# Kernel tuning notes

Hardware: AMD Instinct MI355X
Metric: run time of the kernel (lower is better)

Reference implementation:

```python
import jax, jax.numpy as jnp
import numpy as np

D = 2048       # hidden / input / output width
DEPTH = 9      # infinite_depth (layer default)


def _infinite_layer(x, inf_w, cls_w, cls_b):
    """Faithful vectorized InfiniteNeuralLayer.forward.

    Original per-(sample, j, depth) Python loops build a circulant rotation
    matrix M = cos*I + sin*(shift_down - shift_up) and apply it 3x per depth
    with angles inf_w[depth, j, 0..2]. The rotated state never depends on x,
    so we carry one state row per output index j and scan over the 27 angle
    steps, expressing M @ s as cos*s + sin*(roll(s,1) - roll(s,-1)).
    infinite_biases is unused in the original forward and is omitted.
    """
    dim = x.shape[1]
    classical = x @ cls_w + cls_b                      # [B, dim]
    # angles per j per depth step: (DEPTH, dim_j, 3) -> sequence (DEPTH*3, dim_j)
    angles = jnp.transpose(inf_w[:, :, :3], (0, 2, 1)).reshape(-1, dim)
    init = jnp.full((dim, dim), 1.0 / np.sqrt(dim), dtype=x.dtype)  # [j, state]

    def step(s, a):
        c = jnp.cos(a)[:, None]
        sn = jnp.sin(a)[:, None]
        s_new = c * s + sn * (jnp.roll(s, 1, axis=1) - jnp.roll(s, -1, axis=1))
        return s_new, None

    state, _ = jax.lax.scan(step, init, angles)        # [dim_j, dim]
    p = state[:, 0] ** 2                               # |state[0]|^2 per j
    return jnp.tanh(classical + p[None, :])            # broadcast over batch


def setup_inputs() -> dict:
    key = jax.random.key(0)
    ks = jax.random.split(key, 16)
    s = 0.02  # keep activations in sane range (original uses raw randn)
    f = jax.random.normal
    return {
        "x":      f(ks[0], (2048, D), dtype=jnp.float32),
        "w0":     f(ks[1], (D, D), dtype=jnp.float32) * s,
        "b0":     f(ks[2], (D,), dtype=jnp.float32) * s,
        "w1":     f(ks[3], (D, D), dtype=jnp.float32) * s,
        "b1":     f(ks[4], (D,), dtype=jnp.float32) * s,
        "inf_w1": f(ks[5], (DEPTH, D, D), dtype=jnp.float32),
        "cls_w1": f(ks[6], (D, D), dtype=jnp.float32) * s,
        "cls_b1": f(ks[7], (D,), dtype=jnp.float32) * s,
        "w2":     f(ks[8], (D, D), dtype=jnp.float32) * s,
        "b2":     f(ks[9], (D,), dtype=jnp.float32) * s,
        "inf_w2": f(ks[10], (DEPTH, D, D), dtype=jnp.float32),
        "cls_w2": f(ks[11], (D, D), dtype=jnp.float32) * s,
        "cls_b2": f(ks[12], (D,), dtype=jnp.float32) * s,
        "w3":     f(ks[13], (D, D), dtype=jnp.float32) * s,
        "b3":     f(ks[14], (D,), dtype=jnp.float32) * s,
    }


def reference(x, w0, b0, w1, b1, inf_w1, cls_w1, cls_b1,
              w2, b2, inf_w2, cls_w2, cls_b2, w3, b3):
    h = jax.nn.relu(x @ w0 + b0)
    h = jax.nn.relu(h @ w1 + b1)
    h = _infinite_layer(h, inf_w1, cls_w1, cls_b1)
    h = jax.nn.relu(h @ w2 + b2)
    h = _infinite_layer(h, inf_w2, cls_w2, cls_b2)
    return jax.nn.relu(h @ w3 + b3)
```

## Files before the change

### kernel.cpp

```cpp
#include <hip/hip_runtime.h>
#include <hip/hip_bf16.h>


#define DD 2048
#define DEPTH 9

#define BM 128
#define BN 64
#define BK 32
#define NT (DD / BK)

typedef __attribute__((ext_vector_type(8))) short short8;
typedef __attribute__((ext_vector_type(4))) float f32x4;

__device__ __forceinline__ unsigned short f2bf(float f) {
  unsigned u = __float_as_uint(f);
  u += 0x7FFFu + ((u >> 16) & 1u);
  return (unsigned short)(u >> 16);
}

__global__ __launch_bounds__(256) void prep_kernel(
    const float* __restrict__ w0, const float* __restrict__ w1,
    unsigned short* __restrict__ wts, const float* __restrict__ x,
    unsigned short* __restrict__ xb, const float* __restrict__ infw1,
    const float* __restrict__ infw2, const float* __restrict__ clsb1,
    const float* __restrict__ clsb2, float* __restrict__ padd1,
    float* __restrict__ padd2) {
  int b = blockIdx.x;
  int tid = threadIdx.x;
  if (b < 8192) {
    __shared__ float tile[32][33];
    int z = b >> 12;
    int t = b & 4095;
    const float* src = z ? w1 : w0;
    unsigned short* dst = wts + (size_t)z * DD * DD;
    int bx = (t & 63) * 32;
    int by = (t >> 6) * 32;
    int tx = tid & 31, ty = tid >> 5;
#pragma unroll
    for (int i = ty; i < 32; i += 8)
      tile[i][tx] = src[(size_t)(by + i) * DD + bx + tx];
    __syncthreads();
#pragma unroll
    for (int i = ty; i < 32; i += 8)
      dst[(size_t)(bx + i) * DD + by + tx] = f2bf(tile[tx][i]);
  } else if (b < 12288) {
    int i = (b - 8192) * 256 + tid;
    float4 v = reinterpret_cast<const float4*>(x)[i];
    ushort4 o;
    o.x = f2bf(v.x); o.y = f2bf(v.y); o.z = f2bf(v.z); o.w = f2bf(v.w);
    reinterpret_cast<ushort4*>(xb)[i] = o;
  } else {
    int jj = (b - 12288) * 256 + tid;
    int layer = jj >> 11;
    int j = jj & 2047;
    const float* inf_w = layer ? infw2 : infw1;
    const float* cls_b = layer ? clsb2 : clsb1;
    float* padd = layer ? padd2 : padd1;
    float prod = 1.0f;
#pragma unroll
    for (int d = 0; d < DEPTH; ++d) {
      const float* row = inf_w + ((size_t)d * DD + j) * DD;
      prod *= cosf(row[0]) * cosf(row[1]) * cosf(row[2]);
    }
    padd[j] = cls_b[j] + prod * prod * (1.0f / (float)DD);
  }
}


__device__ __forceinline__ void gload_lds16(const unsigned short* g,
                                            unsigned short* l) {
  __builtin_amdgcn_global_load_lds(
      (const __attribute__((address_space(1))) void*)g,
      (__attribute__((address_space(3))) void*)l, 16, 0, 0);
}

__device__ __forceinline__ void waitv6() {
  asm volatile("s_waitcnt vmcnt(6)" ::: "memory");
}
__device__ __forceinline__ void waitv3() {
  asm volatile("s_waitcnt vmcnt(3)" ::: "memory");
}
__device__ __forceinline__ void waitv0() {
  asm volatile("s_waitcnt vmcnt(0)" ::: "memory");
}

template <int EPI>
__global__ __launch_bounds__(256) void gemm_kernel(
    const unsigned short* __restrict__ A, const unsigned short* __restrict__ Bt,
    const float* __restrict__ bias, unsigned short* __restrict__ Cb,
    float* __restrict__ Cf, const float* __restrict__ tsrc,
    unsigned short* __restrict__ tdst) {
  const int N = DD, K = DD;
  __shared__ __align__(16) unsigned char smem[49152];
  unsigned short* As = (unsigned short*)smem;
  unsigned short* Bs = (unsigned short*)(smem + 4 * BM * BK * 2);

  int tid = threadIdx.x;
  int wid = tid >> 6, lane = tid & 63;
  int wr = wid >> 1, wc = wid & 1;
  int lr = lane & 15;
  int lg = lane >> 4;

  int bid = blockIdx.x;
  int swz = (bid & 7) * 64 + (bid >> 3);
  int bcol = (swz & 31) * BN;
  int brow = (swz >> 5) * BM;

  const unsigned short* Abase = A + (size_t)brow * K;
  const unsigned short* Bbase = Bt + (size_t)bcol * K;

  auto stage = [&](int buf, int tile) {
    int kt = tile * BK;
#pragma unroll
    for (int r = 0; r < 2; ++r) {
      int chunk = r * 256 + tid;
      int row = chunk >> 2;
      int sp = chunk & 3;
      int kof = (sp ^ ((row >> 1) & 3)) * 8;
      gload_lds16(Abase + (size_t)row * K + kt + kof,
                  As + buf * (BM * BK) + (size_t)(r * 256 + wid * 64) * 8);
    }
    {
      int row = tid >> 2;
      int sp = tid & 3;
      int kof = (sp ^ ((row >> 1) & 3)) * 8;
      gload_lds16(Bbase + (size_t)row * K + kt + kof,
                  Bs + buf * (BN * BK) + (size_t)(wid * 64) * 8);
    }
  };

  f32x4 acc[4][2];
#pragma unroll
  for (int i = 0; i < 4; ++i)
#pragma unroll
    for (int j = 0; j < 2; ++j) acc[i][j] = f32x4{0.f, 0.f, 0.f, 0.f};

  auto compute = [&](int buf) {
    short8 a[4], b[2];
#pragma unroll
    for (int mt = 0; mt < 4; ++mt) {
      int row = wr * 64 + mt * 16 + lr;
      int slot = lg ^ ((row >> 1) & 3);
      a[mt] = *reinterpret_cast<const short8*>(
          &As[buf * (BM * BK) + row * BK + slot * 8]);
    }
#pragma unroll
    for (int nt = 0; nt < 2; ++nt) {
      int row = wc * 32 + nt * 16 + lr;
      int slot = lg ^ ((row >> 1) & 3);
      b[nt] = *reinterpret_cast<const short8*>(
          &Bs[buf * (BN * BK) + row * BK + slot * 8]);
    }
    __builtin_amdgcn_s_setprio(1);
#pragma unroll
    for (int mt = 0; mt < 4; ++mt)
#pragma unroll
      for (int nt = 0; nt < 2; ++nt)
        acc[mt][nt] = __builtin_amdgcn_mfma_f32_16x16x32_bf16(
            a[mt], b[nt], acc[mt][nt], 0, 0, 0);
    __builtin_amdgcn_s_setprio(0);
  };

  auto step = [&](int buf, int pf_tile, int wcase) {
    if (wcase == 0) waitv6();
    else if (wcase == 1) waitv3();
    else waitv0();
    __builtin_amdgcn_s_barrier();
    __builtin_amdgcn_sched_barrier(0);
    compute(buf);
    if (pf_tile < NT) stage(pf_tile & 3, pf_tile);
  };

  stage(0, 0); stage(1, 1); stage(2, 2);
#pragma unroll 1
  for (int i = 0; i < 15; ++i) {
    int t = 4 * i;
    step(0, t + 3, 0);
    step(1, t + 4, 0);
    step(2, t + 5, 0);
    step(3, t + 6, 0);
  }
  step(0, 63, 0);
  step(1, NT, 0);
  step(2, NT, 1);
  step(3, NT, 2);

  {
    float* et = reinterpret_cast<float*>(smem);
    __syncthreads();
#pragma unroll
    for (int nt = 0; nt < 2; ++nt) {
      int colb = wc * 32 + nt * 16 + lr;
      float bs = bias[bcol + colb];
#pragma unroll
      for (int mt = 0; mt < 4; ++mt) {
#pragma unroll
        for (int i = 0; i < 4; ++i) {
          int rowb = wr * 64 + mt * 16 + lg * 4 + i;
          float v = acc[mt][nt][i] + bs;
          v = (EPI == 1) ? tanhf(v) : fmaxf(v, 0.0f);
          et[rowb * 68 + colb] = v;
        }
      }
    }
    __syncthreads();
#pragma unroll
    for (int it = 0; it < 4; ++it) {
      int chunk = it * 256 + tid;
      int rowb = chunk >> 3;
      int c8 = (chunk & 7) * 8;
      float4 v0 = *reinterpret_cast<const float4*>(&et[rowb * 68 + c8]);
      float4 v1 = *reinterpret_cast<const float4*>(&et[rowb * 68 + c8 + 4]);
      size_t g = (size_t)(brow + rowb) * N + bcol + c8;
      if (EPI == 2) {
        *reinterpret_cast<float4*>(&Cf[g]) = v0;
        *reinterpret_cast<float4*>(&Cf[g + 4]) = v1;
      } else {
        uint4 o;
        o.x = (unsigned)f2bf(v0.x) | ((unsigned)f2bf(v0.y) << 16);
        o.y = (unsigned)f2bf(v0.z) | ((unsigned)f2bf(v0.w) << 16);
        o.z = (unsigned)f2bf(v1.x) | ((unsigned)f2bf(v1.y) << 16);
        o.w = (unsigned)f2bf(v1.z) | ((unsigned)f2bf(v1.w) << 16);
        *reinterpret_cast<uint4*>(&Cb[g]) = o;
      }
    }
  }

  if (tsrc != nullptr) {
    float* ft = reinterpret_cast<float*>(smem);
    __syncthreads();
#pragma unroll 1
    for (int t2 = 0; t2 < 2; ++t2) {
      int tau = bid * 2 + t2;
      int bx = (tau & 31) * 64;
      int by = (tau >> 5) * 64;
      if (t2) __syncthreads();
#pragma unroll
      for (int it = 0; it < 4; ++it) {
        int idx = it * 256 + tid;
        int r = idx >> 4, c4 = (idx & 15) * 4;
        float4 v = *reinterpret_cast<const float4*>(
            &tsrc[(size_t)(by + r) * DD + bx + c4]);
        ft[r * 65 + c4 + 0] = v.x;
        ft[r * 65 + c4 + 1] = v.y;
        ft[r * 65 + c4 + 2] = v.z;
        ft[r * 65 + c4 + 3] = v.w;
      }
      __syncthreads();
#pragma unroll
      for (int it = 0; it < 4; ++it) {
        int idx = it * 256 + tid;
        int n = idx >> 4, kq = idx & 15;
        ushort4 o;
        o.x = f2bf(ft[(kq * 4 + 0) * 65 + n]);
        o.y = f2bf(ft[(kq * 4 + 1) * 65 + n]);
        o.z = f2bf(ft[(kq * 4 + 2) * 65 + n]);
        o.w = f2bf(ft[(kq * 4 + 3) * 65 + n]);
        *reinterpret_cast<ushort4*>(&tdst[(size_t)(bx + n) * DD + by + kq * 4]) = o;
      }
    }
  }
}


extern "C" void kernel_launch(void* const* d_in, const int* in_sizes, int n_in,
                              void* d_out, int out_size, void* d_ws,
                              size_t ws_size, hipStream_t stream) {
  const float* x     = (const float*)d_in[0];
  const float* w0    = (const float*)d_in[1];
  const float* b0    = (const float*)d_in[2];
  const float* w1    = (const float*)d_in[3];
  const float* b1    = (const float*)d_in[4];
  const float* infw1 = (const float*)d_in[5];
  const float* clsw1 = (const float*)d_in[6];
  const float* clsb1 = (const float*)d_in[7];
  const float* w2    = (const float*)d_in[8];
  const float* b2    = (const float*)d_in[9];
  const float* infw2 = (const float*)d_in[10];
  const float* clsw2 = (const float*)d_in[11];
  const float* clsb2 = (const float*)d_in[12];
  const float* w3    = (const float*)d_in[13];
  const float* b3    = (const float*)d_in[14];
  float* out = (float*)d_out;

  char* ws = (char*)d_ws;
  const size_t MB = 1ull << 20;
  const size_t DDe = (size_t)DD * DD;
  unsigned short* buf0 = (unsigned short*)ws;
  unsigned short* buf1 = (unsigned short*)(ws + 8 * MB);
  unsigned short* wts  = (unsigned short*)(ws + 16 * MB);
  float* padd1 = (float*)(ws + 64 * MB);
  float* padd2 = padd1 + DD;

  prep_kernel<<<12304, 256, 0, stream>>>(w0, w1, wts, x, buf0, infw1, infw2,
                                         clsb1, clsb2, padd1, padd2);

  dim3 gg((DD / BM) * (DD / BN));
  gemm_kernel<0><<<gg, 256, 0, stream>>>(buf0, wts + 0 * DDe, b0,    buf1,
                                         nullptr, clsw1, wts + 2 * DDe);
  gemm_kernel<0><<<gg, 256, 0, stream>>>(buf1, wts + 1 * DDe, b1,    buf0,
                                         nullptr, w2,    wts + 3 * DDe);
  gemm_kernel<1><<<gg, 256, 0, stream>>>(buf0, wts + 2 * DDe, padd1, buf1,
                                         nullptr, clsw2, wts + 4 * DDe);
  gemm_kernel<0><<<gg, 256, 0, stream>>>(buf1, wts + 3 * DDe, b2,    buf0,
                                         nullptr, w3,    wts + 5 * DDe);
  gemm_kernel<1><<<gg, 256, 0, stream>>>(buf0, wts + 4 * DDe, padd2, buf1,
                                         nullptr, nullptr, nullptr);
  gemm_kernel<2><<<gg, 256, 0, stream>>>(buf1, wts + 5 * DDe, b3,    nullptr,
                                         out, nullptr, nullptr);
}
```

Baseline: 221.1 us.

## Load B operand directly into registers, stage only A through LDS

The GEMM now fetches the B tile straight from global memory into per-lane registers with a 3-deep register ring, instead of staging it through LDS. The warp layout changes from 2x2 to 4x1, so each wave covers 32 rows by the full 64 columns, and the accumulator shape becomes 2x4. This is meant to cut LDS traffic, LDS footprint and ds_read instructions for B. The cost is that all four waves load the same B data redundantly from global memory or cache, more registers are used, and the vmcnt wait counts must track the mixed load streams correctly.

Measured after the change: 471.9 us. 2.13x slower.

```diff
diff --git a/kernel.cpp b/kernel.cpp
--- a/kernel.cpp
+++ b/kernel.cpp
@@ -9,6 +9,7 @@
 #define BN 64
 #define BK 32
 #define NT (DD / BK)
+#define ABUF (BM * BK)
 
 typedef __attribute__((ext_vector_type(8))) short short8;
 typedef __attribute__((ext_vector_type(4))) float f32x4;
@@ -75,15 +76,38 @@
       (__attribute__((address_space(3))) void*)l, 16, 0, 0);
 }
 
-__device__ __forceinline__ void waitv6() {
-  asm volatile("s_waitcnt vmcnt(6)" ::: "memory");
-}
-__device__ __forceinline__ void waitv3() {
-  asm volatile("s_waitcnt vmcnt(3)" ::: "memory");
-}
-__device__ __forceinline__ void waitv0() {
-  asm volatile("s_waitcnt vmcnt(0)" ::: "memory");
-}
+#define MFMA_(A_, B_, C_) \
+  __builtin_amdgcn_mfma_f32_16x16x32_bf16(A_, B_, C_, 0, 0, 0)
+
+#define BLOAD(S, tileexpr) do {                                            \
+    const unsigned short* _bp = Blane + (size_t)(tileexpr) * BK;           \
+    _Pragma("unroll")                                                      \
+    for (int _nt = 0; _nt < 4; ++_nt)                                      \
+      breg##S[_nt] = *reinterpret_cast<const short8*>(                     \
+          _bp + (size_t)(_nt * 16) * DD);                                  \
+  } while (0)
+
+#define STEP(BUF, S, LS, t, WC, DO_B, DO_A) do {                           \
+    if ((WC) == 0) asm volatile("s_waitcnt vmcnt(8)" ::: "memory");        \
+    else if ((WC) == 1) asm volatile("s_waitcnt vmcnt(6)" ::: "memory");   \
+    else asm volatile("s_waitcnt vmcnt(0)" ::: "memory");                  \
+    __builtin_amdgcn_s_barrier();                                          \
+    __builtin_amdgcn_sched_barrier(0);                                     \
+    if (DO_B) BLOAD(LS, (t) + 2);                                          \
+    {                                                                      \
+      short8 _a0 = *reinterpret_cast<const short8*>(&As[(BUF)*ABUF + aoff0]); \
+      short8 _a1 = *reinterpret_cast<const short8*>(&As[(BUF)*ABUF + aoff1]); \
+      __builtin_amdgcn_s_setprio(1);                                       \
+      _Pragma("unroll")                                                    \
+      for (int _nt = 0; _nt < 4; ++_nt) {                                  \
+        acc[0][_nt] = MFMA_(_a0, breg##S[_nt], acc[0][_nt]);               \
+        acc[1][_nt] = MFMA_(_a1, breg##S[_nt], acc[1][_nt]);               \
+      }                                                                    \
+      __builtin_amdgcn_s_setprio(0);                                       \
+    }                                                                      \
+    __builtin_amdgcn_sched_barrier(0);                                     \
+    if (DO_A) stageA(((BUF) + 3) & 3, (t) + 3);                            \
+  } while (0)
 
 template <int EPI>
 __global__ __launch_bounds__(256) void gemm_kernel(
@@ -92,13 +116,11 @@
     float* __restrict__ Cf, const float* __restrict__ tsrc,
     unsigned short* __restrict__ tdst) {
   const int N = DD, K = DD;
-  __shared__ __align__(16) unsigned char smem[49152];
+  __shared__ __align__(16) unsigned char smem[36864];
   unsigned short* As = (unsigned short*)smem;
-  unsigned short* Bs = (unsigned short*)(smem + 4 * BM * BK * 2);
 
   int tid = threadIdx.x;
   int wid = tid >> 6, lane = tid & 63;
-  int wr = wid >> 1, wc = wid & 1;
   int lr = lane & 15;
   int lg = lane >> 4;
 
@@ -108,9 +130,9 @@
   int brow = (swz >> 5) * BM;
 
   const unsigned short* Abase = A + (size_t)brow * K;
-  const unsigned short* Bbase = Bt + (size_t)bcol * K;
-
-  auto stage = [&](int buf, int tile) {
+  const unsigned short* Blane = Bt + (size_t)(bcol + lr) * DD + lg * 8;
+
+  auto stageA = [&](int buf, int tile) {
     int kt = tile * BK;
 #pragma unroll
     for (int r = 0; r < 2; ++r) {
@@ -119,85 +141,62 @@
       int sp = chunk & 3;
       int kof = (sp ^ ((row >> 1) & 3)) * 8;
       gload_lds16(Abase + (size_t)row * K + kt + kof,
-                  As + buf * (BM * BK) + (size_t)(r * 256 + wid * 64) * 8);
-    }
-    {
-      int row = tid >> 2;
-      int sp = tid & 3;
-      int kof = (sp ^ ((row >> 1) & 3)) * 8;
-      gload_lds16(Bbase + (size_t)row * K + kt + kof,
-                  Bs + buf * (BN * BK) + (size_t)(wid * 64) * 8);
+                  As + buf * ABUF + (size_t)(r * 256 + wid * 64) * 8);
     }
   };
 
-  f32x4 acc[4][2];
-#pragma unroll
-  for (int i = 0; i < 4; ++i)
-#pragma unroll
-    for (int j = 0; j < 2; ++j) acc[i][j] = f32x4{0.f, 0.f, 0.f, 0.f};
-
-  auto compute = [&](int buf) {
-    short8 a[4], b[2];
-#pragma unroll
-    for (int mt = 0; mt < 4; ++mt) {
-      int row = wr * 64 + mt * 16 + lr;
-      int slot = lg ^ ((row >> 1) & 3);
-      a[mt] = *reinterpret_cast<const short8*>(
-          &As[buf * (BM * BK) + row * BK + slot * 8]);
-    }
-#pragma unroll
-    for (int nt = 0; nt < 2; ++nt) {
-      int row = wc * 32 + nt * 16 + lr;
-      int slot = lg ^ ((row >> 1) & 3);
-      b[nt] = *reinterpret_cast<const short8*>(
-          &Bs[buf * (BN * BK) + row * BK + slot * 8]);
-    }
-    __builtin_amdgcn_s_setprio(1);
-#pragma unroll
-    for (int mt = 0; mt < 4; ++mt)
-#pragma unroll
-      for (int nt = 0; nt < 2; ++nt)
-        acc[mt][nt] = __builtin_amdgcn_mfma_f32_16x16x32_bf16(
-            a[mt], b[nt], acc[mt][nt], 0, 0, 0);
-    __builtin_amdgcn_s_setprio(0);
-  };
-
-  auto step = [&](int buf, int pf_tile, int wcase) {
-    if (wcase == 0) waitv6();
-    else if (wcase == 1) waitv3();
-    else waitv0();
-    __builtin_amdgcn_s_barrier();
-    __builtin_amdgcn_sched_barrier(0);
-    compute(buf);
-    if (pf_tile < NT) stage(pf_tile & 3, pf_tile);
-  };
-
-  stage(0, 0); stage(1, 1); stage(2, 2);
+  int row0 = wid * 32 + lr;
+  int row1 = row0 + 16;
+  int aoff0 = row0 * BK + (lg ^ ((row0 >> 1) & 3)) * 8;
+  int aoff1 = row1 * BK + (lg ^ ((row1 >> 1) & 3)) * 8;
+
+  f32x4 acc[2][4];
+#pragma unroll
+  for (int i = 0; i < 2; ++i)
+#pragma unroll
+    for (int j = 0; j < 4; ++j) acc[i][j] = f32x4{0.f, 0.f, 0.f, 0.f};
+
+  short8 breg0[4], breg1[4], breg2[4];
+
+  stageA(0, 0);
+  BLOAD(0, 0);
+  stageA(1, 1);
+  BLOAD(1, 1);
+  stageA(2, 2);
+
 #pragma unroll 1
-  for (int i = 0; i < 15; ++i) {
-    int t = 4 * i;
-    step(0, t + 3, 0);
-    step(1, t + 4, 0);
-    step(2, t + 5, 0);
-    step(3, t + 6, 0);
+  for (int i = 0; i < 5; ++i) {
+    int t = 12 * i;
+    STEP(0, 0, 2, t + 0, 0, 1, 1);
+    STEP(1, 1, 0, t + 1, 0, 1, 1);
+    STEP(2, 2, 1, t + 2, 0, 1, 1);
+    STEP(3, 0, 2, t + 3, 0, 1, 1);
+    STEP(0, 1, 0, t + 4, 0, 1, 1);
+    STEP(1, 2, 1, t + 5, 0, 1, 1);
+    STEP(2, 0, 2, t + 6, 0, 1, 1);
+    STEP(3, 1, 0, t + 7, 0, 1, 1);
+    STEP(0, 2, 1, t + 8, 0, 1, 1);
+    STEP(1, 0, 2, t + 9, 0, 1, 1);
+    STEP(2, 1, 0, t + 10, 0, 1, 1);
+    STEP(3, 2, 1, t + 11, 0, 1, 1);
   }
-  step(0, 63, 0);
-  step(1, NT, 0);
-  step(2, NT, 1);
-  step(3, NT, 2);
+  STEP(0, 0, 2, 60, 0, 1, 1);
+  STEP(1, 1, 0, 61, 0, 1, 0);
+  STEP(2, 2, 1, 62, 1, 0, 0);
+  STEP(3, 0, 2, 63, 2, 0, 0);
 
   {
     float* et = reinterpret_cast<float*>(smem);
     __syncthreads();
 #pragma unroll
-    for (int nt = 0; nt < 2; ++nt) {
-      int colb = wc * 32 + nt * 16 + lr;
+    for (int nt = 0; nt < 4; ++nt) {
+      int colb = nt * 16 + lr;
       float bs = bias[bcol + colb];
 #pragma unroll
-      for (int mt = 0; mt < 4; ++mt) {
+      for (int mt = 0; mt < 2; ++mt) {
 #pragma unroll
         for (int i = 0; i < 4; ++i) {
-          int rowb = wr * 64 + mt * 16 + lg * 4 + i;
+          int rowb = wid * 32 + mt * 16 + lg * 4 + i;
           float v = acc[mt][nt][i] + bs;
           v = (EPI == 1) ? tanhf(v) : fmaxf(v, 0.0f);
           et[rowb * 68 + colb] = v;
```

## Switch GEMM to single-wave 64x128 tiles without block barriers

Applied to the files above, without the earlier changes.

Restructures the GEMM so each block is one 64-thread wave computing a 64x128 tile with 32 accumulators, replacing the 4-wave 128x64 block. Since only one wave touches LDS, the s_barrier and __syncthreads calls are replaced by vmcnt/lgkmcnt waits, and the prefetch is issued before compute instead of after. Each wave holds more accumulator registers and reuses each loaded fragment more, but occupancy per CU drops and each wave issues more global loads per stage.

Result: slower. 364.7 us (+65.0%).

```diff
diff --git a/kernel.cpp b/kernel.cpp
--- a/kernel.cpp
+++ b/kernel.cpp
@@ -5,10 +5,13 @@
 #define DD 2048
 #define DEPTH 9
 
-#define BM 128
-#define BN 64
+#define BM 64
+#define BN 128
 #define BK 32
 #define NT (DD / BK)
+#define ABUF (BM * BK)
+#define BBUF (BN * BK)
+#define NBUF 4
 
 typedef __attribute__((ext_vector_type(8))) short short8;
 typedef __attribute__((ext_vector_type(4))) float f32x4;
@@ -75,37 +78,25 @@
       (__attribute__((address_space(3))) void*)l, 16, 0, 0);
 }
 
-__device__ __forceinline__ void waitv6() {
-  asm volatile("s_waitcnt vmcnt(6)" ::: "memory");
-}
-__device__ __forceinline__ void waitv3() {
-  asm volatile("s_waitcnt vmcnt(3)" ::: "memory");
-}
-__device__ __forceinline__ void waitv0() {
-  asm volatile("s_waitcnt vmcnt(0)" ::: "memory");
-}
-
 template <int EPI>
-__global__ __launch_bounds__(256) void gemm_kernel(
+__global__ __launch_bounds__(64, 2) void gemm_kernel(
     const unsigned short* __restrict__ A, const unsigned short* __restrict__ Bt,
     const float* __restrict__ bias, unsigned short* __restrict__ Cb,
     float* __restrict__ Cf, const float* __restrict__ tsrc,
     unsigned short* __restrict__ tdst) {
-  const int N = DD, K = DD;
+  const int K = DD;
   __shared__ __align__(16) unsigned char smem[49152];
   unsigned short* As = (unsigned short*)smem;
-  unsigned short* Bs = (unsigned short*)(smem + 4 * BM * BK * 2);
-
-  int tid = threadIdx.x;
-  int wid = tid >> 6, lane = tid & 63;
-  int wr = wid >> 1, wc = wid & 1;
+  unsigned short* Bs = (unsigned short*)(smem + NBUF * ABUF * 2);
+
+  int lane = threadIdx.x;
   int lr = lane & 15;
   int lg = lane >> 4;
 
   int bid = blockIdx.x;
   int swz = (bid & 7) * 64 + (bid >> 3);
-  int bcol = (swz & 31) * BN;
-  int brow = (swz >> 5) * BM;
+  int bcol = (swz & 15) * BN;
+  int brow = (swz >> 4) * BM;
 
   const unsigned short* Abase = A + (size_t)brow * K;
   const unsigned short* Bbase = Bt + (size_t)bcol * K;
@@ -113,63 +104,62 @@
   auto stage = [&](int buf, int tile) {
     int kt = tile * BK;
 #pragma unroll
-    for (int r = 0; r < 2; ++r) {
-      int chunk = r * 256 + tid;
-      int row = chunk >> 2;
-      int sp = chunk & 3;
+    for (int r = 0; r < 4; ++r) {
+      int c = r * 64 + lane;
+      int row = c >> 2, sp = c & 3;
       int kof = (sp ^ ((row >> 1) & 3)) * 8;
       gload_lds16(Abase + (size_t)row * K + kt + kof,
-                  As + buf * (BM * BK) + (size_t)(r * 256 + wid * 64) * 8);
-    }
-    {
-      int row = tid >> 2;
-      int sp = tid & 3;
+                  As + buf * ABUF + r * 512);
+    }
+#pragma unroll
+    for (int r = 0; r < 8; ++r) {
+      int c = r * 64 + lane;
+      int row = c >> 2, sp = c & 3;
       int kof = (sp ^ ((row >> 1) & 3)) * 8;
       gload_lds16(Bbase + (size_t)row * K + kt + kof,
-                  Bs + buf * (BN * BK) + (size_t)(wid * 64) * 8);
+                  Bs + buf * BBUF + r * 512);
     }
   };
 
-  f32x4 acc[4][2];
+  f32x4 acc[4][8];
 #pragma unroll
   for (int i = 0; i < 4; ++i)
 #pragma unroll
-    for (int j = 0; j < 2; ++j) acc[i][j] = f32x4{0.f, 0.f, 0.f, 0.f};
+    for (int j = 0; j < 8; ++j) acc[i][j] = f32x4{0.f, 0.f, 0.f, 0.f};
 
   auto compute = [&](int buf) {
-    short8 a[4], b[2];
+    short8 a[4], b[8];
 #pragma unroll
     for (int mt = 0; mt < 4; ++mt) {
-      int row = wr * 64 + mt * 16 + lr;
+      int row = mt * 16 + lr;
       int slot = lg ^ ((row >> 1) & 3);
       a[mt] = *reinterpret_cast<const short8*>(
-          &As[buf * (BM * BK) + row * BK + slot * 8]);
-    }
-#pragma unroll
-    for (int nt = 0; nt < 2; ++nt) {
-      int row = wc * 32 + nt * 16 + lr;
+          &As[buf * ABUF + row * BK + slot * 8]);
+    }
+#pragma unroll
+    for (int nt = 0; nt < 8; ++nt) {
+      int row = nt * 16 + lr;
       int slot = lg ^ ((row >> 1) & 3);
       b[nt] = *reinterpret_cast<const short8*>(
-          &Bs[buf * (BN * BK) + row * BK + slot * 8]);
+          &Bs[buf * BBUF + row * BK + slot * 8]);
     }
     __builtin_amdgcn_s_setprio(1);
 #pragma unroll
     for (int mt = 0; mt < 4; ++mt)
 #pragma unroll
-      for (int nt = 0; nt < 2; ++nt)
+      for (int nt = 0; nt < 8; ++nt)
         acc[mt][nt] = __builtin_amdgcn_mfma_f32_16x16x32_bf16(
             a[mt], b[nt], acc[mt][nt], 0, 0, 0);
     __builtin_amdgcn_s_setprio(0);
   };
 
-  auto step = [&](int buf, int pf_tile, int wcase) {
-    if (wcase == 0) waitv6();
-    else if (wcase == 1) waitv3();
-    else waitv0();
-    __builtin_amdgcn_s_barrier();
+  auto step = [&](int buf, int pf, int wc) {
+    if (wc == 0) asm volatile("s_waitcnt vmcnt(24)" ::: "memory");
+    else if (wc == 1) asm volatile("s_waitcnt vmcnt(12)" ::: "memory");
+    else asm volatile("s_waitcnt vmcnt(0)" ::: "memory");
     __builtin_amdgcn_sched_barrier(0);
+    if (pf < NT) stage(pf & 3, pf);
     compute(buf);
-    if (pf_tile < NT) stage(pf_tile & 3, pf_tile);
   };
 
   stage(0, 0); stage(1, 1); stage(2, 2);
@@ -188,31 +178,33 @@
 
   {
     float* et = reinterpret_cast<float*>(smem);
-    __syncthreads();
-#pragma unroll
-    for (int nt = 0; nt < 2; ++nt) {
-      int colb = wc * 32 + nt * 16 + lr;
+    asm volatile("s_waitcnt lgkmcnt(0)" ::: "memory");
+    __builtin_amdgcn_sched_barrier(0);
+#pragma unroll
+    for (int nt = 0; nt < 8; ++nt) {
+      int colb = nt * 16 + lr;
       float bs = bias[bcol + colb];
 #pragma unroll
       for (int mt = 0; mt < 4; ++mt) {
 #pragma unroll
         for (int i = 0; i < 4; ++i) {
-          int rowb = wr * 64 + mt * 16 + lg * 4 + i;
+          int rowb = mt * 16 + lg * 4 + i;
           float v = acc[mt][nt][i] + bs;
           v = (EPI == 1) ? tanhf(v) : fmaxf(v, 0.0f);
-          et[rowb * 68 + colb] = v;
+          et[rowb * 132 + colb] = v;
         }
       }
     }
-    __syncthreads();
-#pragma unroll
-    for (int it = 0; it < 4; ++it) {
-      int chunk = it * 256 + tid;
-      int rowb = chunk >> 3;
-      int c8 = (chunk & 7) * 8;
-      float4 v0 = *reinterpret_cast<const float4*>(&et[rowb * 68 + c8]);
-      float4 v1 = *reinterpret_cast<const float4*>(&et[rowb * 68 + c8 + 4]);
-      size_t g = (size_t)(brow + rowb) * N + bcol + c8;
+    asm volatile("s_waitcnt lgkmcnt(0)" ::: "memory");
+    __builtin_amdgcn_sched_barrier(0);
+#pragma unroll
+    for (int it = 0; it < 16; ++it) {
+      int c = it * 64 + lane;
+      int rowb = c >> 4;
+      int c8 = (c & 15) * 8;
+      float4 v0 = *reinterpret_cast<const float4*>(&et[rowb * 132 + c8]);
+      float4 v1 = *reinterpret_cast<const float4*>(&et[rowb * 132 + c8 + 4]);
+      size_t g = (size_t)(brow + rowb) * DD + bcol + c8;
       if (EPI == 2) {
         *reinterpret_cast<float4*>(&Cf[g]) = v0;
         *reinterpret_cast<float4*>(&Cf[g + 4]) = v1;
@@ -229,16 +221,16 @@
 
   if (tsrc != nullptr) {
     float* ft = reinterpret_cast<float*>(smem);
-    __syncthreads();
 #pragma unroll 1
     for (int t2 = 0; t2 < 2; ++t2) {
       int tau = bid * 2 + t2;
       int bx = (tau & 31) * 64;
       int by = (tau >> 5) * 64;
-      if (t2) __syncthreads();
-#pragma unroll
-      for (int it = 0; it < 4; ++it) {
-        int idx = it * 256 + tid;
+      asm volatile("s_waitcnt lgkmcnt(0)" ::: "memory");
+      __builtin_amdgcn_sched_barrier(0);
+#pragma unroll
+      for (int it = 0; it < 16; ++it) {
+        int idx = it * 64 + lane;
         int r = idx >> 4, c4 = (idx & 15) * 4;
         float4 v = *reinterpret_cast<const float4*>(
             &tsrc[(size_t)(by + r) * DD + bx + c4]);
@@ -247,10 +239,11 @@
         ft[r * 65 + c4 + 2] = v.z;
         ft[r * 65 + c4 + 3] = v.w;
       }
-      __syncthreads();
-#pragma unroll
-      for (int it = 0; it < 4; ++it) {
-        int idx = it * 256 + tid;
+      asm volatile("s_waitcnt lgkmcnt(0)" ::: "memory");
+      __builtin_amdgcn_sched_barrier(0);
+#pragma unroll
+      for (int it = 0; it < 16; ++it) {
+        int idx = it * 64 + lane;
         int n = idx >> 4, kq = idx & 15;
         ushort4 o;
         o.x = f2bf(ft[(kq * 4 + 0) * 65 + n]);
@@ -297,16 +290,16 @@
                                          clsb1, clsb2, padd1, padd2);
 
   dim3 gg((DD / BM) * (DD / BN));
-  gemm_kernel<0><<<gg, 256, 0, stream>>>(buf0, wts + 0 * DDe, b0,    buf1,
-                                         nullptr, clsw1, wts + 2 * DDe);
-  gemm_kernel<0><<<gg, 256, 0, stream>>>(buf1, wts + 1 * DDe, b1,    buf0,
-                                         nullptr, w2,    wts + 3 * DDe);
-  gemm_kernel<1><<<gg, 256, 0, stream>>>(buf0, wts + 2 * DDe, padd1, buf1,
-                                         nullptr, clsw2, wts + 4 * DDe);
-  gemm_kernel<0><<<gg, 256, 0, stream>>>(buf1, wts + 3 * DDe, b2,    buf0,
-                                         nullptr, w3,    wts + 5 * DDe);
-  gemm_kernel<1><<<gg, 256, 0, stream>>>(buf0, wts + 4 * DDe, padd2, buf1,
-                                         nullptr, nullptr, nullptr);
-  gemm_kernel<2><<<gg, 256, 0, stream>>>(buf1, wts + 5 * DDe, b3,    nullptr,
-                                         out, nullptr, nullptr);
-}
+  gemm_kernel<0><<<gg, 64, 0, stream>>>(buf0, wts + 0 * DDe, b0,    buf1,
+                                        nullptr, clsw1, wts + 2 * DDe);
+  gemm_kernel<0><<<gg, 64, 0, stream>>>(buf1, wts + 1 * DDe, b1,    buf0,
+                                        nullptr, w2,    wts + 3 * DDe);
+  gemm_kernel<1><<<gg, 64, 0, stream>>>(buf0, wts + 2 * DDe, padd1, buf1,
+                                        nullptr, clsw2, wts + 4 * DDe);
+  gemm_kernel<0><<<gg, 64, 0, stream>>>(buf1, wts + 3 * DDe, b2,    buf0,
+                                        nullptr, w3,    wts + 5 * DDe);
+  gemm_kernel<1><<<gg, 64, 0, stream>>>(buf0, wts + 4 * DDe, padd2, buf1,
+                                        nullptr, nullptr, nullptr);
+  gemm_kernel<2><<<gg, 64, 0, stream>>>(buf1, wts + 5 * DDe, b3,    nullptr,
+                                        out, nullptr, nullptr);
+}
```
